# Kernel optimization log

Hardware: AMD Instinct MI355X
Metric: run time of the kernel (lower is better)

The kernel has to match this reference:

```python
import jax, jax.numpy as jnp
import numpy as np

D_MODEL = 2048
N_HEADS = 16
HEAD_DIM = 128
WINDOW = 256
B, T = 2, 2048
SCALE = float(np.sqrt(HEAD_DIM))


def setup_inputs() -> dict:
    key = jax.random.key(0)
    ks = jax.random.split(key, 5)
    init = 0.02
    x = jax.random.normal(ks[0], (B, T, D_MODEL), dtype=jnp.float32)
    Wq = jax.random.normal(ks[1], (D_MODEL, D_MODEL), dtype=jnp.float32) * init
    Wk = jax.random.normal(ks[2], (D_MODEL, D_MODEL), dtype=jnp.float32) * init
    Wv = jax.random.normal(ks[3], (D_MODEL, D_MODEL), dtype=jnp.float32) * init
    Wo = jax.random.normal(ks[4], (D_MODEL, D_MODEL), dtype=jnp.float32) * init
    return {"x": x, "Wq": Wq, "Wk": Wk, "Wv": Wv, "Wo": Wo}


def _allowed_mask():
    # [H, T, T] bool: global (even) heads -> causal; local (odd) heads -> causal band of WINDOW
    idx = jnp.arange(T)
    causal = idx[None, :] <= idx[:, None]                      # [T, T]
    band = idx[None, :] >= (idx[:, None] - WINDOW + 1)         # [T, T]
    is_global = (jnp.arange(N_HEADS) % 2) == 0                 # [H]
    return causal[None] & (is_global[:, None, None] | band[None])


def reference(x, Wq, Wk, Wv, Wo):
    # projections (nn.Linear: y = x @ W.T), reshape to [B, H, T, D]
    def proj(W):
        return (x @ W.T).reshape(B, T, N_HEADS, HEAD_DIM).transpose(0, 2, 1, 3)

    q, k, v = proj(Wq), proj(Wk), proj(Wv)
    scores = jnp.einsum("bhtd,bhsd->bhts", q, k) / SCALE       # [B, H, T, T]
    allowed = _allowed_mask()                                  # [H, T, T]
    neg_inf = jnp.asarray(-jnp.inf, dtype=scores.dtype)
    scores = jnp.where(allowed[None], scores, neg_inf)
    attn = jax.nn.softmax(scores, axis=-1)
    out = jnp.einsum("bhts,bhsd->bhtd", attn, v)               # [B, H, T, D]
    concat = out.transpose(0, 2, 1, 3).reshape(B, T, N_HEADS * HEAD_DIM)
    return concat @ Wo.T
```

## Files before the change

### kernel.cpp

```cpp
#include <hip/hip_runtime.h>

typedef __attribute__((ext_vector_type(4))) float f32x4;
typedef __attribute__((ext_vector_type(8))) short bf16x8;
typedef __attribute__((ext_vector_type(4))) unsigned short u16x4;
typedef unsigned short u16;

#define MFMA16(a, b, c) __builtin_amdgcn_mfma_f32_16x16x32_bf16((a), (b), (c), 0, 0, 0)

#define T_SEQ 2048
#define DMODEL 2048
#define NHEADS 16
#define HDIM 128
#define WINDOW 256
#define MROWS 4096
#define SC 0.08838834764831845f

__device__ __forceinline__ u16 f2bf(float f) {
  union { float f; unsigned u; } v; v.f = f;
  return (u16)((v.u + 0x7FFFu + ((v.u >> 16) & 1u)) >> 16);
}
__device__ __forceinline__ float bf2f(u16 u) {
  union { unsigned u; float f; } v; v.u = ((unsigned)u) << 16;
  return v.f;
}
__device__ __forceinline__ void gl_lds16(const u16* g, u16* l) {
  __builtin_amdgcn_global_load_lds((const __attribute__((address_space(1))) void*)(g),
                                   (__attribute__((address_space(3))) void*)(l), 16, 0, 0);
}

#define BAR __builtin_amdgcn_s_barrier()
#define FEN asm volatile("" ::: "memory")
#define VMC3 asm volatile("s_waitcnt vmcnt(3)" ::: "memory")
#define VMC2 asm volatile("s_waitcnt vmcnt(2)" ::: "memory")
#define VMC0 asm volatile("s_waitcnt vmcnt(0)" ::: "memory")

__global__ __launch_bounds__(256) void convert_all(const float* __restrict__ x,
                                                   const float* __restrict__ wq,
                                                   const float* __restrict__ wk,
                                                   const float* __restrict__ wv,
                                                   const float* __restrict__ wo,
                                                   u16* __restrict__ dst) {
  const size_t NX = (size_t)MROWS * DMODEL;
  const size_t NW = (size_t)DMODEL * DMODEL;
  const size_t chunks = (NX + 4 * NW) / 8;
  for (size_t ci = (size_t)blockIdx.x * 256 + threadIdx.x; ci < chunks;
       ci += (size_t)gridDim.x * 256) {
    const size_t off = ci * 8;
    const float* src;
    size_t so;
    if (off < NX) { src = x; so = off; }
    else {
      size_t rem = off - NX;
      if (rem < NW) { src = wq; so = rem; }
      else if (rem < 2 * NW) { src = wk; so = rem - NW; }
      else if (rem < 3 * NW) { src = wv; so = rem - 2 * NW; }
      else { src = wo; so = rem - 3 * NW; }
    }
    f32x4 a = *(const f32x4*)&src[so];
    f32x4 b = *(const f32x4*)&src[so + 4];
    bf16x8 o;
#pragma unroll
    for (int j = 0; j < 4; ++j) { o[j] = (short)f2bf(a[j]); o[j + 4] = (short)f2bf(b[j]); }
    *(bf16x8*)&dst[off] = o;
  }
}

__global__ __launch_bounds__(512, 2) void gemm_qkv(const u16* __restrict__ A,
                                                   const u16* __restrict__ W,
                                                   u16* __restrict__ qk,
                                                   u16* __restrict__ vt) {
  __shared__ u16 lds[57344];
  const int tid = threadIdx.x, w = tid >> 6, lane = tid & 63;
  const int wm = w >> 2, wn = w & 3;
  const int fr = lane & 15, g = lane >> 4, g4 = g * 4;

  const int xcd = blockIdx.x & 7, bi = blockIdx.x >> 3;
  const int mt = bi >> 2, nt = xcd * 4 + (bi & 3);
  const int m0 = mt * 256, n0 = nt * 192;

  const int xs0 = (g ^ (fr & 7)) * 8;
  const int xs1 = xs0 ^ 32;
  const int aRow = wm * 128 + fr;
  const int bRow = wn * 48 + fr;

  const int sr = tid >> 3;
  const int scc = ((tid & 7) ^ (sr & 7)) * 8;
  const u16* pA0  = A + (size_t)(m0 + sr) * DMODEL + scc;
  const u16* pA1  = A + (size_t)(m0 + 64 + sr) * DMODEL + scc;
  const u16* pB0  = W + (size_t)(n0 + sr) * DMODEL + scc;
  const u16* pB0b = W + (size_t)(n0 + 64 + sr) * DMODEL + scc;
  const u16* pB1  = W + (size_t)(n0 + 128 + sr) * DMODEL + scc;

#define SAH(h, t, c)                                                                   \
  { gl_lds16(pA0 + (size_t)(h) * 128 * DMODEL + (t) * 64,                              \
             &lds[(c) * 16384 + (h) * 8192 + w * 512]);                                \
    gl_lds16(pA1 + (size_t)(h) * 128 * DMODEL + (t) * 64,                              \
             &lds[(c) * 16384 + (h) * 8192 + 4096 + w * 512]); }
#define SBH0(t, c)                                                                     \
  { gl_lds16(pB0 + (size_t)(t) * 64, &lds[32768 + (c) * 12288 + w * 512]);             \
    gl_lds16(pB0b + (size_t)(t) * 64, &lds[32768 + (c) * 12288 + 4096 + w * 512]); }
#define SBH1(t, c)                                                                     \
  { gl_lds16(pB1 + (size_t)(t) * 64, &lds[32768 + (c) * 12288 + 8192 + w * 512]); }

#define RD_AL(c)                                                                       \
  { _Pragma("unroll") for (int m_ = 0; m_ < 4; ++m_) {                                 \
      af[m_][0] = *(const bf16x8*)&lds[(c) * 16384 + (aRow + m_ * 16) * 64 + xs0];     \
      af[m_][1] = *(const bf16x8*)&lds[(c) * 16384 + (aRow + m_ * 16) * 64 + xs1]; } }
#define RD_AH(c)                                                                       \
  { _Pragma("unroll") for (int m_ = 0; m_ < 4; ++m_) {                                 \
      af[m_][0] = *(const bf16x8*)&lds[(c) * 16384 + (aRow + 64 + m_ * 16) * 64 + xs0];\
      af[m_][1] = *(const bf16x8*)&lds[(c) * 16384 + (aRow + 64 + m_ * 16) * 64 + xs1]; } }
#define RD_B(c)                                                                        \
  { _Pragma("unroll") for (int n_ = 0; n_ < 3; ++n_) {                                 \
      bfr[n_][0] = *(const bf16x8*)&lds[32768 + (c) * 12288 + (bRow + n_ * 16) * 64 + xs0]; \
      bfr[n_][1] = *(const bf16x8*)&lds[32768 + (c) * 12288 + (bRow + n_ * 16) * 64 + xs1]; } }

#define MMQ(MB)                                                                        \
  { __builtin_amdgcn_s_setprio(1);                                                    \
    _Pragma("unroll") for (int kc_ = 0; kc_ < 2; ++kc_)                                \
      _Pragma("unroll") for (int m_ = 0; m_ < 4; ++m_)                                 \
        _Pragma("unroll") for (int n_ = 0; n_ < 3; ++n_)                               \
          acc[(MB) + m_][n_] = MFMA16(af[m_][kc_], bfr[n_][kc_], acc[(MB) + m_][n_]);  \
    __builtin_amdgcn_s_setprio(0); }

  bf16x8 af[4][2], bfr[3][2];
  f32x4 acc[8][3];
#pragma unroll
  for (int i = 0; i < 8; ++i)
#pragma unroll
    for (int j = 0; j < 3; ++j) acc[i][j] = (f32x4){0.f, 0.f, 0.f, 0.f};

  SAH(0, 0, 0); SAH(1, 0, 0);
  SBH0(0, 0); SBH1(0, 0);
  SBH0(1, 1); SBH1(1, 1);
  VMC3; BAR;

#pragma unroll 1
  for (int i = 0; i < 15; ++i) {
    const int t0 = 2 * i;
    RD_AL(0); RD_B(0); SAH(0, t0 + 1, 1); SAH(1, t0 + 1, 1);
    FEN; BAR; MMQ(0); FEN; BAR;
    RD_AH(0); SBH0(t0 + 2, 0); SBH1(t0 + 2, 0);
    VMC3; BAR; MMQ(4); FEN; BAR;
    RD_AL(1); RD_B(1); SAH(0, t0 + 2, 0); SAH(1, t0 + 2, 0);
    FEN; BAR; MMQ(0); FEN; BAR;
    RD_AH(1); SBH0(t0 + 3, 1); SBH1(t0 + 3, 1);
    VMC3; BAR; MMQ(4); FEN; BAR;
  }
  RD_AL(0); RD_B(0); SAH(0, 31, 1); SAH(1, 31, 1);
  FEN; BAR; MMQ(0); FEN; BAR;
  RD_AH(0);
  VMC0; BAR; MMQ(4); FEN; BAR;
  RD_AL(1); RD_B(1);
  FEN; BAR; MMQ(0); FEN; BAR;
  RD_AH(1);
  FEN; BAR; MMQ(4);

#pragma unroll
  for (int mi = 0; mi < 8; ++mi)
#pragma unroll
    for (int ni = 0; ni < 3; ++ni) {
      const int row0 = m0 + wm * 128 + mi * 16 + g4;
      const int cg = n0 + wn * 48 + ni * 16 + fr;
      if (cg < 2 * DMODEL) {
#pragma unroll
        for (int r = 0; r < 4; ++r)
          qk[(size_t)(row0 + r) * (2 * DMODEL) + cg] = f2bf(acc[mi][ni][r]);
      } else {
        const int cc = cg - 2 * DMODEL;
        const int hh = cc >> 7, d = cc & 127;
        const int bb = row0 >> 11, tl = row0 & 2047;
        u16x4 w4;
#pragma unroll
        for (int r = 0; r < 4; ++r) w4[r] = f2bf(acc[mi][ni][r]);
        *(u16x4*)&vt[((size_t)(bb * NHEADS + hh) * HDIM + d) * T_SEQ + tl] = w4;
      }
    }
#undef SAH
#undef SBH0
#undef SBH1
#undef RD_AL
#undef RD_AH
#undef RD_B
#undef MMQ
}

__global__ __launch_bounds__(512, 2) void gemm_out(const u16* __restrict__ A,
                                                   const u16* __restrict__ W0,
                                                   float* __restrict__ outf) {
  __shared__ u16 lds2[49152];
  const int tid = threadIdx.x, w = tid >> 6, lane = tid & 63;
  const int wm = w >> 2, wn = w & 3;
  const int fr = lane & 15, g = lane >> 4, g4 = g * 4;

  const int xcd = blockIdx.x & 7, bi = blockIdx.x >> 3;
  const int mt = bi >> 1, nt = xcd * 2 + (bi & 1);
  const int m0 = mt * 256, n0 = nt * 128;

  const int xs0 = (g ^ (fr & 7)) * 8;
  const int xs1 = xs0 ^ 32;
  const int aRow = wm * 128 + fr;
  const int bRow = wn * 32 + fr;

  const int sr = tid >> 3;
  const int scc = ((tid & 7) ^ (sr & 7)) * 8;
  const u16* pA0  = A + (size_t)(m0 + sr) * DMODEL + scc;
  const u16* pA1  = A + (size_t)(m0 + 64 + sr) * DMODEL + scc;
  const u16* pB0  = W0 + (size_t)(n0 + sr) * DMODEL + scc;
  const u16* pB0b = W0 + (size_t)(n0 + 64 + sr) * DMODEL + scc;

#define S2A(h, t, c)                                                                   \
  { gl_lds16(pA0 + (size_t)(h) * 128 * DMODEL + (t) * 64,                              \
             &lds2[(c) * 16384 + (h) * 8192 + w * 512]);                               \
    gl_lds16(pA1 + (size_t)(h) * 128 * DMODEL + (t) * 64,                              \
             &lds2[(c) * 16384 + (h) * 8192 + 4096 + w * 512]); }
#define S2B(t, c)                                                                      \
  { gl_lds16(pB0 + (size_t)(t) * 64, &lds2[32768 + (c) * 8192 + w * 512]);             \
    gl_lds16(pB0b + (size_t)(t) * 64, &lds2[32768 + (c) * 8192 + 4096 + w * 512]); }

#define R2AL(c)                                                                        \
  { _Pragma("unroll") for (int m_ = 0; m_ < 4; ++m_) {                                 \
      af[m_][0] = *(const bf16x8*)&lds2[(c) * 16384 + (aRow + m_ * 16) * 64 + xs0];    \
      af[m_][1] = *(const bf16x8*)&lds2[(c) * 16384 + (aRow + m_ * 16) * 64 + xs1]; } }
#define R2AH(c)                                                                        \
  { _Pragma("unroll") for (int m_ = 0; m_ < 4; ++m_) {                                 \
      af[m_][0] = *(const bf16x8*)&lds2[(c) * 16384 + (aRow + 64 + m_ * 16) * 64 + xs0]; \
      af[m_][1] = *(const bf16x8*)&lds2[(c) * 16384 + (aRow + 64 + m_ * 16) * 64 + xs1]; } }
#define R2B(c)                                                                         \
  { _Pragma("unroll") for (int n_ = 0; n_ < 2; ++n_) {                                 \
      bfr[n_][0] = *(const bf16x8*)&lds2[32768 + (c) * 8192 + (bRow + n_ * 16) * 64 + xs0]; \
      bfr[n_][1] = *(const bf16x8*)&lds2[32768 + (c) * 8192 + (bRow + n_ * 16) * 64 + xs1]; } }

#define M2(MB)                                                                         \
  { __builtin_amdgcn_s_setprio(1);                                                    \
    _Pragma("unroll") for (int kc_ = 0; kc_ < 2; ++kc_)                                \
      _Pragma("unroll") for (int m_ = 0; m_ < 4; ++m_)                                 \
        _Pragma("unroll") for (int n_ = 0; n_ < 2; ++n_)                               \
          acc[(MB) + m_][n_] = MFMA16(af[m_][kc_], bfr[n_][kc_], acc[(MB) + m_][n_]);  \
    __builtin_amdgcn_s_setprio(0); }

  bf16x8 af[4][2], bfr[2][2];
  f32x4 acc[8][2];
#pragma unroll
  for (int i = 0; i < 8; ++i)
#pragma unroll
    for (int j = 0; j < 2; ++j) acc[i][j] = (f32x4){0.f, 0.f, 0.f, 0.f};

  S2A(0, 0, 0); S2A(1, 0, 0);
  S2B(0, 0);
  S2B(1, 1);
  VMC2; BAR;

#pragma unroll 1
  for (int i = 0; i < 15; ++i) {
    const int t0 = 2 * i;
    R2AL(0); R2B(0); S2A(0, t0 + 1, 1); S2A(1, t0 + 1, 1);
    FEN; BAR; M2(0); FEN; BAR;
    R2AH(0); S2B(t0 + 2, 0);
    VMC2; BAR; M2(4); FEN; BAR;
    R2AL(1); R2B(1); S2A(0, t0 + 2, 0); S2A(1, t0 + 2, 0);
    FEN; BAR; M2(0); FEN; BAR;
    R2AH(1); S2B(t0 + 3, 1);
    VMC2; BAR; M2(4); FEN; BAR;
  }
  R2AL(0); R2B(0); S2A(0, 31, 1); S2A(1, 31, 1);
  FEN; BAR; M2(0); FEN; BAR;
  R2AH(0);
  VMC0; BAR; M2(4); FEN; BAR;
  R2AL(1); R2B(1);
  FEN; BAR; M2(0); FEN; BAR;
  R2AH(1);
  FEN; BAR; M2(4);

#pragma unroll
  for (int mi = 0; mi < 8; ++mi)
#pragma unroll
    for (int ni = 0; ni < 2; ++ni) {
      const int row0 = m0 + wm * 128 + mi * 16 + g4;
      const int c = n0 + wn * 32 + ni * 16 + fr;
#pragma unroll
      for (int r = 0; r < 4; ++r)
        outf[(size_t)(row0 + r) * DMODEL + c] = acc[mi][ni][r];
    }
#undef S2A
#undef S2B
#undef R2AL
#undef R2AH
#undef R2B
#undef M2
}

#define QB 128
#define KVB 64

__global__ __launch_bounds__(512, 4) void attn_kernel(const u16* __restrict__ qk,
                                                      const u16* __restrict__ vt,
                                                      u16* __restrict__ op,
                                                      u16* __restrict__ pO,
                                                      float* __restrict__ pm,
                                                      float* __restrict__ pl) {
  __shared__ u16 lds[40960];

  const int bx = blockIdx.x, h = blockIdx.y, b = blockIdx.z;
  const bool isglobal = (h & 1) == 0;
  int qt, klo, khi, part = 0;
  bool partial = false;
  if (isglobal) {
    if (bx < 16) {
      qt = 15 - (bx >> 1);
      part = bx & 1;
      partial = true;
      if (part == 0) { klo = 0; khi = 15; } else { klo = 16; khi = 2 * qt + 1; }
    } else {
      qt = 23 - bx;
      klo = 0; khi = 2 * qt + 1;
    }
  } else {
    if (bx >= 16) return;
    qt = 15 - bx;
    const int lo_ = qt * QB - (WINDOW - 1);
    klo = lo_ > 0 ? (lo_ >> 6) : 0;
    khi = 2 * qt + 1;
  }

  const int tid = threadIdx.x, wave = tid >> 6, lane = tid & 63;
  const int fr = lane & 15, g = lane >> 4, g4 = g * 4;
  const int xk = fr & 7;
  const int q0 = qt * QB;
  const size_t baseq = (size_t)b * T_SEQ * (2 * DMODEL) + (size_t)h * HDIM;
  const size_t basek = baseq + DMODEL;
  const size_t basev = (size_t)(b * NHEADS + h) * HDIM * T_SEQ;
  const size_t baseo = (size_t)b * T_SEQ * DMODEL + (size_t)h * HDIM;

  bf16x8 qf[4];
  {
    const int qrow = q0 + wave * 16 + fr;
#pragma unroll
    for (int ds = 0; ds < 4; ++ds)
      qf[ds] = *(const bf16x8*)&qk[baseq + (size_t)qrow * (2 * DMODEL) + ds * 32 + g * 8];
  }

  float mrun = -1e30f, lrun = 0.f;
  f32x4 o[8];
#pragma unroll
  for (int dt = 0; dt < 8; ++dt) o[dt] = (f32x4){0.f, 0.f, 0.f, 0.f};

  const int j0 = wave * 2, j1 = wave * 2 + 1;
  const int gi0 = j0 * 64 + lane, gi1 = j1 * 64 + lane;
  const int kr0 = gi0 >> 4, kc0 = (gi0 & 15) ^ (kr0 & 7);
  const int kr1 = gi1 >> 4, kc1 = (gi1 & 15) ^ (kr1 & 7);
  const u16* pK0 = qk + basek + (size_t)kr0 * (2 * DMODEL) + kc0 * 8;
  const u16* pK1 = qk + basek + (size_t)kr1 * (2 * DMODEL) + kc1 * 8;
  const int d0 = gi0 >> 3, vs0 = (gi0 & 7) ^ (d0 & 7);
  const int d1 = gi1 >> 3, vs1 = (gi1 & 7) ^ (d1 & 7);
  const u16* pV0 = vt + basev + (size_t)d0 * T_SEQ + vs0 * 8;
  const u16* pV1 = vt + basev + (size_t)d1 * T_SEQ + vs1 * 8;

#define STAGE(KT, c)                                                                   \
  { gl_lds16(pK0 + (size_t)(KT) * (KVB * 2 * DMODEL), &lds[(c) * 8192 + j0 * 512]);    \
    gl_lds16(pK1 + (size_t)(KT) * (KVB * 2 * DMODEL), &lds[(c) * 8192 + j1 * 512]);    \
    gl_lds16(pV0 + (KT) * KVB, &lds[16384 + (c) * 8192 + j0 * 512]);                   \
    gl_lds16(pV1 + (KT) * KVB, &lds[16384 + (c) * 8192 + j1 * 512]); }

  u16* Pw = &lds[32768 + wave * 1024];
  const int qg = q0 + wave * 16 + fr;

  STAGE(klo, klo & 1);
  VMC0; BAR;

  for (int kt = klo; kt <= khi; ++kt) {
    const int c = kt & 1;
    const bool more = kt < khi;
    if (more) STAGE(kt + 1, c ^ 1);
    const u16* Kc = &lds[c * 8192];
    const u16* Vc = &lds[16384 + c * 8192];

    f32x4 s[4];
    __builtin_amdgcn_s_setprio(1);
#pragma unroll
    for (int kk = 0; kk < 4; ++kk) {
      f32x4 a = (f32x4){0.f, 0.f, 0.f, 0.f};
#pragma unroll
      for (int ds = 0; ds < 4; ++ds) {
        const int r = kk * 16 + fr;
        bf16x8 kf = *(const bf16x8*)&Kc[r * 128 + (((ds * 4 + g) ^ xk) << 3)];
        a = MFMA16(kf, qf[ds], a);
      }
      s[kk] = a;
    }
    __builtin_amdgcn_s_setprio(0);

    float sv[16];
    float pmax = -1e30f;
#pragma unroll
    for (int kk = 0; kk < 4; ++kk)
#pragma unroll
      for (int reg = 0; reg < 4; ++reg) {
        const int cg = kt * KVB + kk * 16 + g4 + reg;
        const bool allowed = (cg <= qg) && (isglobal || cg >= qg - (WINDOW - 1));
        const float v = allowed ? s[kk][reg] : -1e30f;
        sv[kk * 4 + reg] = v;
        pmax = fmaxf(pmax, v);
      }
    pmax = fmaxf(pmax, __shfl_xor(pmax, 16, 64));
    pmax = fmaxf(pmax, __shfl_xor(pmax, 32, 64));
    const bool resc = !__all(pmax - mrun <= 90.5f);
    float fac = 1.f;
    if (resc) {
      const float nm = fmaxf(mrun, pmax);
      fac = __expf((mrun - nm) * SC);
      mrun = nm;
    }
    float rs = 0.f;
    u16 pb[16];
#pragma unroll
    for (int i = 0; i < 16; ++i) {
      const float p = (sv[i] > -5e29f) ? __expf((sv[i] - mrun) * SC) : 0.f;
      rs += p;
      pb[i] = f2bf(p);
    }
    rs += __shfl_xor(rs, 16, 64);
    rs += __shfl_xor(rs, 32, 64);
    lrun = lrun * fac + rs;

#pragma unroll
    for (int kk = 0; kk < 4; ++kk) {
      u16x4 wv;
      wv[0] = pb[kk * 4]; wv[1] = pb[kk * 4 + 1]; wv[2] = pb[kk * 4 + 2]; wv[3] = pb[kk * 4 + 3];
      *(u16x4*)&Pw[fr * 64 + (((2 * kk + (g >> 1)) ^ xk) << 3) + (g & 1) * 4] = wv;
    }

    if (resc) {
      float ff[4];
#pragma unroll
      for (int r = 0; r < 4; ++r) ff[r] = __shfl(fac, g4 + r, 64);
#pragma unroll
      for (int dt = 0; dt < 8; ++dt)
#pragma unroll
        for (int r = 0; r < 4; ++r) o[dt][r] *= ff[r];
    }

    bf16x8 pf0 = *(const bf16x8*)&Pw[fr * 64 + ((g ^ xk) << 3)];
    bf16x8 pf1 = *(const bf16x8*)&Pw[fr * 64 + (((4 + g) ^ xk) << 3)];
    __builtin_amdgcn_s_setprio(1);
#pragma unroll
    for (int dt = 0; dt < 8; ++dt) {
      const int d = dt * 16 + fr;
      bf16x8 vf0 = *(const bf16x8*)&Vc[d * 64 + ((g ^ xk) << 3)];
      bf16x8 vf1 = *(const bf16x8*)&Vc[d * 64 + (((4 + g) ^ xk) << 3)];
      o[dt] = MFMA16(pf0, vf0, o[dt]);
      o[dt] = MFMA16(pf1, vf1, o[dt]);
    }
    __builtin_amdgcn_s_setprio(0);

    FEN;
    VMC0;
    BAR;
  }

  if (!partial) {
    const float inv = 1.0f / lrun;
    float iv[4];
#pragma unroll
    for (int r = 0; r < 4; ++r) iv[r] = __shfl(inv, g4 + r, 64);
#pragma unroll
    for (int r = 0; r < 4; ++r) {
      const int qrow = q0 + wave * 16 + g4 + r;
#pragma unroll
      for (int dt = 0; dt < 8; ++dt)
        op[baseo + (size_t)qrow * DMODEL + dt * 16 + fr] = f2bf(o[dt][r] * iv[r]);
    }
  } else {
    const int sidx = (((b * 8 + (h >> 1)) * 8 + (qt - 8)) << 1) + part;
    const size_t sb = (size_t)sidx * QB;
#pragma unroll
    for (int r = 0; r < 4; ++r) {
      const size_t row = sb + wave * 16 + g4 + r;
#pragma unroll
      for (int dt = 0; dt < 8; ++dt)
        pO[row * HDIM + dt * 16 + fr] = f2bf(o[dt][r]);
    }
    if (lane < 16) {
      pm[sb + wave * 16 + lane] = mrun;
      pl[sb + wave * 16 + lane] = lrun;
    }
  }
#undef STAGE
}

__global__ __launch_bounds__(256) void merge_kernel(const u16* __restrict__ pO,
                                                    const float* __restrict__ pm,
                                                    const float* __restrict__ pl,
                                                    u16* __restrict__ op) {
  const int x = blockIdx.x;
  const int qt8 = x & 7, eh = (x >> 3) & 7, b = x >> 6;
  const int h = eh * 2, qt = 8 + qt8;
  const int s0 = x * 2, s1 = s0 + 1;

  for (int i = 0; i < 8; ++i) {
    const int vidx = threadIdx.x + i * 256;
    const int row = vidx >> 4, d8 = (vidx & 15) * 8;
    const float m0 = pm[s0 * QB + row], m1 = pm[s1 * QB + row];
    const float l0 = pl[s0 * QB + row], l1 = pl[s1 * QB + row];
    const float m = fmaxf(m0, m1);
    const float w0 = __expf((m0 - m) * SC), w1 = __expf((m1 - m) * SC);
    const float inv = 1.0f / (l0 * w0 + l1 * w1);
    bf16x8 a = *(const bf16x8*)&pO[((size_t)s0 * QB + row) * HDIM + d8];
    bf16x8 c = *(const bf16x8*)&pO[((size_t)s1 * QB + row) * HDIM + d8];
    bf16x8 r;
#pragma unroll
    for (int j = 0; j < 8; ++j)
      r[j] = (short)f2bf((bf2f((u16)a[j]) * w0 + bf2f((u16)c[j]) * w1) * inv);
    *(bf16x8*)&op[((size_t)(b * T_SEQ + qt * QB + row)) * DMODEL + h * HDIM + d8] = r;
  }
}

extern "C" void kernel_launch(void* const* d_in, const int* in_sizes, int n_in,
                              void* d_out, int out_size, void* d_ws, size_t ws_size,
                              hipStream_t stream) {
  (void)in_sizes; (void)n_in; (void)out_size; (void)ws_size;
  const float* x  = (const float*)d_in[0];
  const float* Wq = (const float*)d_in[1];
  const float* Wk = (const float*)d_in[2];
  const float* Wv = (const float*)d_in[3];
  const float* Wo = (const float*)d_in[4];

  const size_t NX = (size_t)MROWS * DMODEL;
  const size_t NW = (size_t)DMODEL * DMODEL;
  u16* ws  = (u16*)d_ws;
  u16* xb  = ws;
  u16* wqb = ws + NX;
  u16* wkb = wqb + NW;
  u16* wvb = wkb + NW;
  u16* wob = wvb + NW;
  u16* qkb = wob + NW;
  u16* vtb = qkb + (size_t)MROWS * 2 * DMODEL;

  u16*   pO = wqb;
  float* pm = (float*)(wqb + (size_t)256 * QB * HDIM);
  float* pl = pm + 256 * QB;

  convert_all<<<2048, 256, 0, stream>>>(x, Wq, Wk, Wv, Wo, ws);

  gemm_qkv<<<512, 512, 0, stream>>>(xb, wqb, qkb, vtb);

  attn_kernel<<<dim3(24, NHEADS, 2), 512, 0, stream>>>(qkb, vtb, xb, pO, pm, pl);

  merge_kernel<<<128, 256, 0, stream>>>(pO, pm, pl, xb);

  gemm_out<<<256, 512, 0, stream>>>(xb, wob, (float*)d_out);
}
```

Baseline: 250.1 us.

## Split global-head attention into 8-tile KV chunks and fold softmax scale into Q

Global-head query tiles are now split into up to four KV chunks of 8 tiles each, in place of the old two-way split that covered only the upper half of tiles. This spreads causal work more evenly across many more workgroups, and the merge kernel is generalised to combine 2-4 partials per tile. The softmax scale is also folded into Q at the QKV GEMM epilogue, which removes the per-element multiply in the exp path and changes the rescale threshold accordingly. The cost is more partial-output traffic, extra early-exit blocks, and a larger merge step.

New measurement: 260.8 us. 4.3% more time.

```diff
diff --git a/kernel.cpp b/kernel.cpp
--- a/kernel.cpp
+++ b/kernel.cpp
@@ -163,9 +163,10 @@
       const int row0 = m0 + wm * 128 + mi * 16 + g4;
       const int cg = n0 + wn * 48 + ni * 16 + fr;
       if (cg < 2 * DMODEL) {
+        const float qs = (cg < DMODEL) ? SC : 1.0f;
 #pragma unroll
         for (int r = 0; r < 4; ++r)
-          qk[(size_t)(row0 + r) * (2 * DMODEL) + cg] = f2bf(acc[mi][ni][r]);
+          qk[(size_t)(row0 + r) * (2 * DMODEL) + cg] = f2bf(acc[mi][ni][r] * qs);
       } else {
         const int cc = cg - 2 * DMODEL;
         const int hh = cc >> 7, d = cc & 127;
@@ -303,17 +304,20 @@
 
   const int bx = blockIdx.x, h = blockIdx.y, b = blockIdx.z;
   const bool isglobal = (h & 1) == 0;
-  int qt, klo, khi, part = 0;
+  int qt, klo, khi, sidx = 0;
   bool partial = false;
   if (isglobal) {
-    if (bx < 16) {
-      qt = 15 - (bx >> 1);
-      part = bx & 1;
-      partial = true;
-      if (part == 0) { klo = 0; khi = 15; } else { klo = 16; khi = 2 * qt + 1; }
-    } else {
-      qt = 23 - bx;
-      klo = 0; khi = 2 * qt + 1;
+    qt = 15 - (bx >> 2);
+    const int ci = bx & 3;
+    const int n = 2 * qt + 2;
+    const int nc = (n + 7) >> 3;
+    if (ci >= nc) return;
+    klo = ci * 8;
+    khi = min(klo + 7, 2 * qt + 1);
+    partial = nc > 1;
+    if (partial) {
+      const int base = (qt < 8) ? (qt - 4) * 2 : (qt < 12 ? 8 + (qt - 8) * 3 : 20 + (qt - 12) * 4);
+      sidx = (b * 8 + (h >> 1)) * 36 + base + ci;
     }
   } else {
     if (bx >= 16) return;
@@ -404,18 +408,18 @@
       }
     pmax = fmaxf(pmax, __shfl_xor(pmax, 16, 64));
     pmax = fmaxf(pmax, __shfl_xor(pmax, 32, 64));
-    const bool resc = !__all(pmax - mrun <= 90.5f);
+    const bool resc = !__all(pmax - mrun <= 8.0f);
     float fac = 1.f;
     if (resc) {
       const float nm = fmaxf(mrun, pmax);
-      fac = __expf((mrun - nm) * SC);
+      fac = __expf(mrun - nm);
       mrun = nm;
     }
     float rs = 0.f;
     u16 pb[16];
 #pragma unroll
     for (int i = 0; i < 16; ++i) {
-      const float p = (sv[i] > -5e29f) ? __expf((sv[i] - mrun) * SC) : 0.f;
+      const float p = (sv[i] > -5e29f) ? __expf(sv[i] - mrun) : 0.f;
       rs += p;
       pb[i] = f2bf(p);
     }
@@ -471,7 +475,6 @@
         op[baseo + (size_t)qrow * DMODEL + dt * 16 + fr] = f2bf(o[dt][r] * iv[r]);
     }
   } else {
-    const int sidx = (((b * 8 + (h >> 1)) * 8 + (qt - 8)) << 1) + part;
     const size_t sb = (size_t)sidx * QB;
 #pragma unroll
     for (int r = 0; r < 4; ++r) {
@@ -493,24 +496,35 @@
                                                     const float* __restrict__ pl,
                                                     u16* __restrict__ op) {
   const int x = blockIdx.x;
-  const int qt8 = x & 7, eh = (x >> 3) & 7, b = x >> 6;
-  const int h = eh * 2, qt = 8 + qt8;
-  const int s0 = x * 2, s1 = s0 + 1;
+  const int qtm4 = x % 12, beh = x / 12;
+  const int eh = beh & 7, b = beh >> 3;
+  const int h = eh * 2, qt = 4 + qtm4;
+  const int nc = (qt < 8) ? 2 : (qt < 12 ? 3 : 4);
+  const int base = (qt < 8) ? (qt - 4) * 2 : (qt < 12 ? 8 + (qt - 8) * 3 : 20 + (qt - 12) * 4);
+  const int s0 = beh * 36 + base;
 
   for (int i = 0; i < 8; ++i) {
     const int vidx = threadIdx.x + i * 256;
     const int row = vidx >> 4, d8 = (vidx & 15) * 8;
-    const float m0 = pm[s0 * QB + row], m1 = pm[s1 * QB + row];
-    const float l0 = pl[s0 * QB + row], l1 = pl[s1 * QB + row];
-    const float m = fmaxf(m0, m1);
-    const float w0 = __expf((m0 - m) * SC), w1 = __expf((m1 - m) * SC);
-    const float inv = 1.0f / (l0 * w0 + l1 * w1);
-    bf16x8 a = *(const bf16x8*)&pO[((size_t)s0 * QB + row) * HDIM + d8];
-    bf16x8 c = *(const bf16x8*)&pO[((size_t)s1 * QB + row) * HDIM + d8];
+    float mv[4], lv[4], wv[4];
+    float mm = -1e30f;
+    for (int c = 0; c < nc; ++c) {
+      mv[c] = pm[(size_t)(s0 + c) * QB + row];
+      lv[c] = pl[(size_t)(s0 + c) * QB + row];
+      mm = fmaxf(mm, mv[c]);
+    }
+    float lsum = 0.f;
+    for (int c = 0; c < nc; ++c) { wv[c] = __expf(mv[c] - mm); lsum += lv[c] * wv[c]; }
+    const float inv = 1.0f / lsum;
+    float a8[8] = {0.f, 0.f, 0.f, 0.f, 0.f, 0.f, 0.f, 0.f};
+    for (int c = 0; c < nc; ++c) {
+      bf16x8 a = *(const bf16x8*)&pO[((size_t)(s0 + c) * QB + row) * HDIM + d8];
+#pragma unroll
+      for (int j = 0; j < 8; ++j) a8[j] += bf2f((u16)a[j]) * wv[c];
+    }
     bf16x8 r;
 #pragma unroll
-    for (int j = 0; j < 8; ++j)
-      r[j] = (short)f2bf((bf2f((u16)a[j]) * w0 + bf2f((u16)c[j]) * w1) * inv);
+    for (int j = 0; j < 8; ++j) r[j] = (short)f2bf(a8[j] * inv);
     *(bf16x8*)&op[((size_t)(b * T_SEQ + qt * QB + row)) * DMODEL + h * HDIM + d8] = r;
   }
 }
@@ -537,16 +551,16 @@
   u16* vtb = qkb + (size_t)MROWS * 2 * DMODEL;
 
   u16*   pO = wqb;
-  float* pm = (float*)(wqb + (size_t)256 * QB * HDIM);
-  float* pl = pm + 256 * QB;
+  float* pm = (float*)(wqb + (size_t)576 * QB * HDIM);
+  float* pl = pm + 576 * QB;
 
   convert_all<<<2048, 256, 0, stream>>>(x, Wq, Wk, Wv, Wo, ws);
 
   gemm_qkv<<<512, 512, 0, stream>>>(xb, wqb, qkb, vtb);
 
-  attn_kernel<<<dim3(24, NHEADS, 2), 512, 0, stream>>>(qkb, vtb, xb, pO, pm, pl);
-
-  merge_kernel<<<128, 256, 0, stream>>>(pO, pm, pl, xb);
+  attn_kernel<<<dim3(64, NHEADS, 2), 512, 0, stream>>>(qkb, vtb, xb, pO, pm, pl);
+
+  merge_kernel<<<192, 256, 0, stream>>>(pO, pm, pl, xb);
 
   gemm_out<<<256, 512, 0, stream>>>(xb, wob, (float*)d_out);
 }
```

## Store K/V head-contiguous and fold softmax scale into Q in QKV epilogue

Applied to the files above, without the earlier changes.

The QKV GEMM epilogue now writes Q pre-multiplied by the softmax scale, K into a per-head [T, D] contiguous buffer, and V into per-head 64-token tiles laid out [tile][d][t]. Each attention K/V stage then reads one contiguous 16 KB block instead of strided rows, and the per-element scale multiply in the exp path is removed (the rescale threshold is adjusted to the new units). In exchange, the K stores in the epilogue become scalar strided writes, and rounding Q after scaling slightly changes numerics.

Result: no change. 246.7 us (median of 2 runs) (-1.3%).

```diff
diff --git a/kernel.cpp b/kernel.cpp
--- a/kernel.cpp
+++ b/kernel.cpp
@@ -67,8 +67,9 @@
 
 __global__ __launch_bounds__(512, 2) void gemm_qkv(const u16* __restrict__ A,
                                                    const u16* __restrict__ W,
-                                                   u16* __restrict__ qk,
-                                                   u16* __restrict__ vt) {
+                                                   u16* __restrict__ qb,
+                                                   u16* __restrict__ kb,
+                                                   u16* __restrict__ vb) {
   __shared__ u16 lds[57344];
   const int tid = threadIdx.x, w = tid >> 6, lane = tid & 63;
   const int wm = w >> 2, wn = w & 3;
@@ -162,18 +163,26 @@
     for (int ni = 0; ni < 3; ++ni) {
       const int row0 = m0 + wm * 128 + mi * 16 + g4;
       const int cg = n0 + wn * 48 + ni * 16 + fr;
-      if (cg < 2 * DMODEL) {
+      const int bb = row0 >> 11, tl = row0 & 2047;
+      if (cg < DMODEL) {
 #pragma unroll
         for (int r = 0; r < 4; ++r)
-          qk[(size_t)(row0 + r) * (2 * DMODEL) + cg] = f2bf(acc[mi][ni][r]);
+          qb[(size_t)(row0 + r) * DMODEL + cg] = f2bf(acc[mi][ni][r] * SC);
+      } else if (cg < 2 * DMODEL) {
+        const int cc = cg - DMODEL;
+        const int hh = cc >> 7, d = cc & 127;
+        const size_t kbase = (size_t)(bb * NHEADS + hh) * T_SEQ * HDIM;
+#pragma unroll
+        for (int r = 0; r < 4; ++r)
+          kb[kbase + (size_t)(tl + r) * HDIM + d] = f2bf(acc[mi][ni][r]);
       } else {
         const int cc = cg - 2 * DMODEL;
         const int hh = cc >> 7, d = cc & 127;
-        const int bb = row0 >> 11, tl = row0 & 2047;
         u16x4 w4;
 #pragma unroll
         for (int r = 0; r < 4; ++r) w4[r] = f2bf(acc[mi][ni][r]);
-        *(u16x4*)&vt[((size_t)(bb * NHEADS + hh) * HDIM + d) * T_SEQ + tl] = w4;
+        *(u16x4*)&vb[(size_t)(bb * NHEADS + hh) * T_SEQ * HDIM + (size_t)(tl >> 6) * 8192 +
+                     d * 64 + (tl & 63)] = w4;
       }
     }
 #undef SAH
@@ -293,8 +302,9 @@
 #define QB 128
 #define KVB 64
 
-__global__ __launch_bounds__(512, 4) void attn_kernel(const u16* __restrict__ qk,
-                                                      const u16* __restrict__ vt,
+__global__ __launch_bounds__(512, 4) void attn_kernel(const u16* __restrict__ qb,
+                                                      const u16* __restrict__ kb,
+                                                      const u16* __restrict__ vb,
                                                       u16* __restrict__ op,
                                                       u16* __restrict__ pO,
                                                       float* __restrict__ pm,
@@ -327,9 +337,8 @@
   const int fr = lane & 15, g = lane >> 4, g4 = g * 4;
   const int xk = fr & 7;
   const int q0 = qt * QB;
-  const size_t baseq = (size_t)b * T_SEQ * (2 * DMODEL) + (size_t)h * HDIM;
-  const size_t basek = baseq + DMODEL;
-  const size_t basev = (size_t)(b * NHEADS + h) * HDIM * T_SEQ;
+  const int bh = b * NHEADS + h;
+  const size_t basek = (size_t)bh * T_SEQ * HDIM;
   const size_t baseo = (size_t)b * T_SEQ * DMODEL + (size_t)h * HDIM;
 
   bf16x8 qf[4];
@@ -337,7 +346,8 @@
     const int qrow = q0 + wave * 16 + fr;
 #pragma unroll
     for (int ds = 0; ds < 4; ++ds)
-      qf[ds] = *(const bf16x8*)&qk[baseq + (size_t)qrow * (2 * DMODEL) + ds * 32 + g * 8];
+      qf[ds] = *(const bf16x8*)&qb[(size_t)b * T_SEQ * DMODEL + (size_t)qrow * DMODEL +
+                                   (size_t)h * HDIM + ds * 32 + g * 8];
   }
 
   float mrun = -1e30f, lrun = 0.f;
@@ -349,18 +359,18 @@
   const int gi0 = j0 * 64 + lane, gi1 = j1 * 64 + lane;
   const int kr0 = gi0 >> 4, kc0 = (gi0 & 15) ^ (kr0 & 7);
   const int kr1 = gi1 >> 4, kc1 = (gi1 & 15) ^ (kr1 & 7);
-  const u16* pK0 = qk + basek + (size_t)kr0 * (2 * DMODEL) + kc0 * 8;
-  const u16* pK1 = qk + basek + (size_t)kr1 * (2 * DMODEL) + kc1 * 8;
+  const u16* pK0 = kb + basek + (size_t)kr0 * HDIM + kc0 * 8;
+  const u16* pK1 = kb + basek + (size_t)kr1 * HDIM + kc1 * 8;
   const int d0 = gi0 >> 3, vs0 = (gi0 & 7) ^ (d0 & 7);
   const int d1 = gi1 >> 3, vs1 = (gi1 & 7) ^ (d1 & 7);
-  const u16* pV0 = vt + basev + (size_t)d0 * T_SEQ + vs0 * 8;
-  const u16* pV1 = vt + basev + (size_t)d1 * T_SEQ + vs1 * 8;
+  const u16* pV0 = vb + basek + (size_t)d0 * 64 + vs0 * 8;
+  const u16* pV1 = vb + basek + (size_t)d1 * 64 + vs1 * 8;
 
 #define STAGE(KT, c)                                                                   \
-  { gl_lds16(pK0 + (size_t)(KT) * (KVB * 2 * DMODEL), &lds[(c) * 8192 + j0 * 512]);    \
-    gl_lds16(pK1 + (size_t)(KT) * (KVB * 2 * DMODEL), &lds[(c) * 8192 + j1 * 512]);    \
-    gl_lds16(pV0 + (KT) * KVB, &lds[16384 + (c) * 8192 + j0 * 512]);                   \
-    gl_lds16(pV1 + (KT) * KVB, &lds[16384 + (c) * 8192 + j1 * 512]); }
+  { gl_lds16(pK0 + (size_t)(KT) * 8192, &lds[(c) * 8192 + j0 * 512]);                  \
+    gl_lds16(pK1 + (size_t)(KT) * 8192, &lds[(c) * 8192 + j1 * 512]);                  \
+    gl_lds16(pV0 + (size_t)(KT) * 8192, &lds[16384 + (c) * 8192 + j0 * 512]);          \
+    gl_lds16(pV1 + (size_t)(KT) * 8192, &lds[16384 + (c) * 8192 + j1 * 512]); }
 
   u16* Pw = &lds[32768 + wave * 1024];
   const int qg = q0 + wave * 16 + fr;
@@ -404,18 +414,18 @@
       }
     pmax = fmaxf(pmax, __shfl_xor(pmax, 16, 64));
     pmax = fmaxf(pmax, __shfl_xor(pmax, 32, 64));
-    const bool resc = !__all(pmax - mrun <= 90.5f);
+    const bool resc = !__all(pmax - mrun <= 8.0f);
     float fac = 1.f;
     if (resc) {
       const float nm = fmaxf(mrun, pmax);
-      fac = __expf((mrun - nm) * SC);
+      fac = __expf(mrun - nm);
       mrun = nm;
     }
     float rs = 0.f;
     u16 pb[16];
 #pragma unroll
     for (int i = 0; i < 16; ++i) {
-      const float p = (sv[i] > -5e29f) ? __expf((sv[i] - mrun) * SC) : 0.f;
+      const float p = (sv[i] > -5e29f) ? __expf(sv[i] - mrun) : 0.f;
       rs += p;
       pb[i] = f2bf(p);
     }
@@ -503,7 +513,7 @@
     const float m0 = pm[s0 * QB + row], m1 = pm[s1 * QB + row];
     const float l0 = pl[s0 * QB + row], l1 = pl[s1 * QB + row];
     const float m = fmaxf(m0, m1);
-    const float w0 = __expf((m0 - m) * SC), w1 = __expf((m1 - m) * SC);
+    const float w0 = __expf(m0 - m), w1 = __expf(m1 - m);
     const float inv = 1.0f / (l0 * w0 + l1 * w1);
     bf16x8 a = *(const bf16x8*)&pO[((size_t)s0 * QB + row) * HDIM + d8];
     bf16x8 c = *(const bf16x8*)&pO[((size_t)s1 * QB + row) * HDIM + d8];
@@ -533,8 +543,9 @@
   u16* wkb = wqb + NW;
   u16* wvb = wkb + NW;
   u16* wob = wvb + NW;
-  u16* qkb = wob + NW;
-  u16* vtb = qkb + (size_t)MROWS * 2 * DMODEL;
+  u16* qbb = wob + NW;
+  u16* kbb = qbb + NX;
+  u16* vbb = kbb + NX;
 
   u16*   pO = wqb;
   float* pm = (float*)(wqb + (size_t)256 * QB * HDIM);
@@ -542,9 +553,9 @@
 
   convert_all<<<2048, 256, 0, stream>>>(x, Wq, Wk, Wv, Wo, ws);
 
-  gemm_qkv<<<512, 512, 0, stream>>>(xb, wqb, qkb, vtb);
-
-  attn_kernel<<<dim3(24, NHEADS, 2), 512, 0, stream>>>(qkb, vtb, xb, pO, pm, pl);
+  gemm_qkv<<<512, 512, 0, stream>>>(xb, wqb, qbb, kbb, vbb);
+
+  attn_kernel<<<dim3(24, NHEADS, 2), 512, 0, stream>>>(qbb, kbb, vbb, xb, pO, pm, pl);
 
   merge_kernel<<<128, 256, 0, stream>>>(pO, pm, pl, xb);
 
```
